# Performance work log

Measured on AMD Instinct MI355X. Metric: run time of the kernel, lower is better.

## Reference

```python
import jax, jax.numpy as jnp
import numpy as np
from jax import lax

EPS = 1e-7  # keras K.epsilon()
DN = ('NHWC', 'HWIO', 'NHWC')


def _box_avg(z, k):
    """Depthwise k x k box filter with SAME padding, scaled by 1/(k*k*C).
    Matches tf.nn.depthwise_conv2d with a ones/(k*k*C) kernel, implemented
    separably (two 1D convs) for efficiency."""
    C = z.shape[-1]
    scale = 1.0 / (k * k * C)  # note: keras code divides by full kernel size incl. C
    kh = jnp.ones((k, 1, 1, C), z.dtype)
    kw = jnp.ones((1, k, 1, C), z.dtype)
    z = lax.conv_general_dilated(z, kh, (1, 1), 'SAME',
                                 dimension_numbers=DN, feature_group_count=C)
    z = lax.conv_general_dilated(z, kw, (1, 1), 'SAME',
                                 dimension_numbers=DN, feature_group_count=C)
    return z * scale


def setup_inputs() -> dict:
    key = jax.random.key(0)
    x = jax.random.normal(key, (8, 1024, 1024, 2), dtype=jnp.float32)
    return {"x": x, "filter_size": 61}


def reference(x, filter_size):
    k = int(filter_size)
    # norm_method == 'std':
    out = x - _box_avg(x, k)                       # local mean-subtract
    c1 = _box_avg(out, k)
    c2 = _box_avg(out * out, k)
    std = jnp.sqrt(c2 - c1 * c1) + EPS             # local window std
    return out / std
```

## Files before the change

### kernel.cpp

```cpp
#include <hip/hip_runtime.h>
#include <math.h>

#define NB 8
#define HH 1024
#define WW 1024
#define CC 2
#define RAD 30
#define KS 61
#define ROWSZ (WW * CC)
#define IMGSZ (HH * ROWSZ)
#define STR (ROWSZ / 2)
#define NCOL2 (NB * STR)
#define VSEGH 64
#define VNSEG (HH / VSEGH)
#define EPSV 1e-7f
#define SCALEV (1.0f / (float)(KS * KS * CC))

__global__ __launch_bounds__(256) void vbox_kernel(const float* __restrict__ in,
                                                   float* __restrict__ out) {
    int tid = blockIdx.x * 256 + threadIdx.x;
    int col = tid & (NCOL2 - 1);
    int seg = tid >> 13;
    int n = col / STR;
    int wc = col & (STR - 1);
    const float2* ip = (const float2*)(in + (size_t)n * IMGSZ) + wc;
    float2* op = (float2*)(out + (size_t)n * IMGSZ) + wc;
    int h0 = seg * VSEGH;
    float Sx = 0.f, Sy = 0.f;
    int lo = h0 - RAD; if (lo < 0) lo = 0;
    int hiex = h0 + RAD;
    int h = lo;
    for (; h + 4 <= hiex; h += 4) {
        float2 v0 = ip[(h + 0) * STR];
        float2 v1 = ip[(h + 1) * STR];
        float2 v2 = ip[(h + 2) * STR];
        float2 v3 = ip[(h + 3) * STR];
        Sx += v0.x + v1.x + v2.x + v3.x;
        Sy += v0.y + v1.y + v2.y + v3.y;
    }
    for (; h < hiex; ++h) { float2 v = ip[h * STR]; Sx += v.x; Sy += v.y; }
    for (int ho = h0; ho < h0 + VSEGH; ho += 4) {
        float2 a[4], b[4];
        #pragma unroll
        for (int i = 0; i < 4; ++i) {
            int ha = ho + i + RAD;
            a[i] = (ha < HH) ? ip[ha * STR] : make_float2(0.f, 0.f);
        }
        #pragma unroll
        for (int i = 0; i < 4; ++i) {
            int hb = ho + i - RAD;
            b[i] = (hb >= 0) ? ip[hb * STR] : make_float2(0.f, 0.f);
        }
        #pragma unroll
        for (int i = 0; i < 4; ++i) {
            Sx += a[i].x; Sy += a[i].y;
            op[(ho + i) * STR] = make_float2(Sx, Sy);
            Sx -= b[i].x; Sy -= b[i].y;
        }
    }
}

__global__ __launch_bounds__(256) void vbox2_kernel(const float* __restrict__ in,
                                                    float* __restrict__ o1,
                                                    float* __restrict__ o2) {
    int tid = blockIdx.x * 256 + threadIdx.x;
    int col = tid & (NCOL2 - 1);
    int seg = tid >> 13;
    int n = col / STR;
    int wc = col & (STR - 1);
    const float2* ip = (const float2*)(in + (size_t)n * IMGSZ) + wc;
    float2* p1 = (float2*)(o1 + (size_t)n * IMGSZ) + wc;
    float2* p2 = (float2*)(o2 + (size_t)n * IMGSZ) + wc;
    int h0 = seg * VSEGH;
    float Sx = 0.f, Sy = 0.f, Qx = 0.f, Qy = 0.f;
    int lo = h0 - RAD; if (lo < 0) lo = 0;
    int hiex = h0 + RAD;
    int h = lo;
    for (; h + 4 <= hiex; h += 4) {
        float2 v0 = ip[(h + 0) * STR];
        float2 v1 = ip[(h + 1) * STR];
        float2 v2 = ip[(h + 2) * STR];
        float2 v3 = ip[(h + 3) * STR];
        Sx += v0.x + v1.x + v2.x + v3.x;
        Sy += v0.y + v1.y + v2.y + v3.y;
        Qx += v0.x * v0.x + v1.x * v1.x + v2.x * v2.x + v3.x * v3.x;
        Qy += v0.y * v0.y + v1.y * v1.y + v2.y * v2.y + v3.y * v3.y;
    }
    for (; h < hiex; ++h) {
        float2 v = ip[h * STR];
        Sx += v.x; Sy += v.y; Qx += v.x * v.x; Qy += v.y * v.y;
    }
    for (int ho = h0; ho < h0 + VSEGH; ho += 4) {
        float2 a[4], b[4];
        #pragma unroll
        for (int i = 0; i < 4; ++i) {
            int ha = ho + i + RAD;
            a[i] = (ha < HH) ? ip[ha * STR] : make_float2(0.f, 0.f);
        }
        #pragma unroll
        for (int i = 0; i < 4; ++i) {
            int hb = ho + i - RAD;
            b[i] = (hb >= 0) ? ip[hb * STR] : make_float2(0.f, 0.f);
        }
        #pragma unroll
        for (int i = 0; i < 4; ++i) {
            Sx += a[i].x; Sy += a[i].y;
            Qx += a[i].x * a[i].x; Qy += a[i].y * a[i].y;
            p1[(ho + i) * STR] = make_float2(Sx, Sy);
            p2[(ho + i) * STR] = make_float2(Qx, Qy);
            Sx -= b[i].x; Sy -= b[i].y;
            Qx -= b[i].x * b[i].x; Qy -= b[i].y * b[i].y;
        }
    }
}

__device__ inline float wave_incl_scan(float v) {
    int lane = threadIdx.x & 63;
    #pragma unroll
    for (int d = 1; d < 64; d <<= 1) {
        float o = __shfl_up(v, d, 64);
        if (lane >= d) v += o;
    }
    return v;
}

__global__ __launch_bounds__(256) void hbox_sub_kernel(const float* __restrict__ vsum,
                                                       const float* __restrict__ x,
                                                       float* __restrict__ out) {
    __shared__ float ch[2][WW];
    __shared__ float wtot[4];
    int t = threadIdx.x;
    size_t g = (size_t)blockIdx.x * ROWSZ;
    const float2* vrow = (const float2*)(vsum + g);
    #pragma unroll
    for (int i = 0; i < 4; ++i) {
        int w = t + 256 * i;
        float2 v = vrow[w];
        ch[0][w] = v.x; ch[1][w] = v.y;
    }
    __syncthreads();
    int c = t >> 7, j = t & 127, base = j * 8;
    float v[8]; float run = 0.f;
    #pragma unroll
    for (int i = 0; i < 8; ++i) { run += ch[c][base + i]; v[i] = run; }
    float incl = wave_incl_scan(run);
    int wid = t >> 6;
    if ((t & 63) == 63) wtot[wid] = incl;
    __syncthreads();
    float off = incl - run;
    if (wid & 1) off += wtot[wid - 1];
    #pragma unroll
    for (int i = 0; i < 8; ++i) ch[c][base + i] = off + v[i];
    __syncthreads();
    #pragma unroll
    for (int i = 0; i < 8; ++i) {
        int e = t + 256 * i;
        int w = e >> 1, cc2 = e & 1;
        int hi = w + RAD; if (hi > WW - 1) hi = WW - 1;
        float s = ch[cc2][hi];
        int lo2 = w - RAD - 1;
        if (lo2 >= 0) s -= ch[cc2][lo2];
        out[g + e] = x[g + e] - SCALEV * s;
    }
}

__global__ __launch_bounds__(256) void hbox_final_kernel(const float* __restrict__ s1v,
                                                         const float* __restrict__ s2v,
                                                         float* __restrict__ out) {
    __shared__ float ch[4][WW];
    int t = threadIdx.x;
    size_t g = (size_t)blockIdx.x * ROWSZ;
    const float2* arow = (const float2*)(s1v + g);
    const float2* brow = (const float2*)(s2v + g);
    #pragma unroll
    for (int i = 0; i < 4; ++i) {
        int w = t + 256 * i;
        float2 a = arow[w]; ch[0][w] = a.x; ch[1][w] = a.y;
        float2 b = brow[w]; ch[2][w] = b.x; ch[3][w] = b.y;
    }
    __syncthreads();
    int a = t >> 6, j = t & 63, base = j * 16;
    float v[16]; float run = 0.f;
    #pragma unroll
    for (int i = 0; i < 16; ++i) { run += ch[a][base + i]; v[i] = run; }
    float incl = wave_incl_scan(run);
    float off = incl - run;
    #pragma unroll
    for (int i = 0; i < 16; ++i) ch[a][base + i] = off + v[i];
    __syncthreads();
    #pragma unroll
    for (int i = 0; i < 8; ++i) {
        int e = t + 256 * i;
        int w = e >> 1, cc2 = e & 1;
        int hi = w + RAD; if (hi > WW - 1) hi = WW - 1;
        int lo2 = w - RAD - 1;
        float s1 = ch[cc2][hi];
        float s2 = ch[2 + cc2][hi];
        if (lo2 >= 0) { s1 -= ch[cc2][lo2]; s2 -= ch[2 + cc2][lo2]; }
        float c1 = SCALEV * s1;
        float c2 = SCALEV * s2;
        float var = c2 - c1 * c1;
        float stdv = sqrtf(fmaxf(var, 0.f)) + EPSV;
        out[g + e] = out[g + e] / stdv;
    }
}

extern "C" void kernel_launch(void* const* d_in, const int* in_sizes, int n_in,
                              void* d_out, int out_size, void* d_ws, size_t ws_size,
                              hipStream_t stream) {
    const float* x = (const float*)d_in[0];
    float* out = (float*)d_out;
    float* wsf = (float*)d_ws;
    float* V1 = wsf;
    float* V3 = wsf + (size_t)NB * IMGSZ;

    vbox_kernel<<<(NCOL2 * VNSEG) / 256, 256, 0, stream>>>(x, V1);
    hbox_sub_kernel<<<NB * HH, 256, 0, stream>>>(V1, x, out);
    vbox2_kernel<<<(NCOL2 * VNSEG) / 256, 256, 0, stream>>>(out, V1, V3);
    hbox_final_kernel<<<NB * HH, 256, 0, stream>>>(V1, V3, out);
}
```

Measured before the change: 239.9 us.

## Vectorize box-filter passes to float4 and pad shared memory to avoid conflicts

The vertical running-sum kernels now use float4 accesses, so each thread handles four floats. Segments are shortened to 32 rows, which keeps thread count similar and adds more warmup overhead per segment. Interior segments get a branch-free path with no boundary checks. The horizontal scan kernels load and store float4 and pad their shared-memory rows (one extra slot per 8) to reduce bank conflicts; this adds index arithmetic and replaces the interleaved access pattern.

```diff
diff --git a/kernel.cpp b/kernel.cpp
--- a/kernel.cpp
+++ b/kernel.cpp
@@ -9,53 +9,84 @@
 #define KS 61
 #define ROWSZ (WW * CC)
 #define IMGSZ (HH * ROWSZ)
-#define STR (ROWSZ / 2)
-#define NCOL2 (NB * STR)
-#define VSEGH 64
+#define STR4 (ROWSZ / 4)
+#define NCOL4 (NB * STR4)
+#define VSEGH 32
 #define VNSEG (HH / VSEGH)
 #define EPSV 1e-7f
 #define SCALEV (1.0f / (float)(KS * KS * CC))
+#define PDW (WW + WW / 8)
+#define PD(i) ((i) + ((i) >> 3))
+
+__device__ __forceinline__ float4 f4add(float4 a, float4 b) {
+    return make_float4(a.x + b.x, a.y + b.y, a.z + b.z, a.w + b.w);
+}
+__device__ __forceinline__ float4 f4sub(float4 a, float4 b) {
+    return make_float4(a.x - b.x, a.y - b.y, a.z - b.z, a.w - b.w);
+}
+__device__ __forceinline__ float4 f4fma(float4 a, float4 b, float4 c) {
+    return make_float4(fmaf(a.x, b.x, c.x), fmaf(a.y, b.y, c.y),
+                       fmaf(a.z, b.z, c.z), fmaf(a.w, b.w, c.w));
+}
 
 __global__ __launch_bounds__(256) void vbox_kernel(const float* __restrict__ in,
                                                    float* __restrict__ out) {
     int tid = blockIdx.x * 256 + threadIdx.x;
-    int col = tid & (NCOL2 - 1);
-    int seg = tid >> 13;
-    int n = col / STR;
-    int wc = col & (STR - 1);
-    const float2* ip = (const float2*)(in + (size_t)n * IMGSZ) + wc;
-    float2* op = (float2*)(out + (size_t)n * IMGSZ) + wc;
+    int col = tid & (NCOL4 - 1);
+    int seg = tid >> 12;
+    int n = col >> 9;
+    int w4 = col & (STR4 - 1);
+    const float4* ip = (const float4*)(in + (size_t)n * IMGSZ) + w4;
+    float4* op = (float4*)(out + (size_t)n * IMGSZ) + w4;
     int h0 = seg * VSEGH;
-    float Sx = 0.f, Sy = 0.f;
+    float4 S = make_float4(0.f, 0.f, 0.f, 0.f);
     int lo = h0 - RAD; if (lo < 0) lo = 0;
     int hiex = h0 + RAD;
     int h = lo;
     for (; h + 4 <= hiex; h += 4) {
-        float2 v0 = ip[(h + 0) * STR];
-        float2 v1 = ip[(h + 1) * STR];
-        float2 v2 = ip[(h + 2) * STR];
-        float2 v3 = ip[(h + 3) * STR];
-        Sx += v0.x + v1.x + v2.x + v3.x;
-        Sy += v0.y + v1.y + v2.y + v3.y;
-    }
-    for (; h < hiex; ++h) { float2 v = ip[h * STR]; Sx += v.x; Sy += v.y; }
-    for (int ho = h0; ho < h0 + VSEGH; ho += 4) {
-        float2 a[4], b[4];
-        #pragma unroll
-        for (int i = 0; i < 4; ++i) {
-            int ha = ho + i + RAD;
-            a[i] = (ha < HH) ? ip[ha * STR] : make_float2(0.f, 0.f);
-        }
-        #pragma unroll
-        for (int i = 0; i < 4; ++i) {
-            int hb = ho + i - RAD;
-            b[i] = (hb >= 0) ? ip[hb * STR] : make_float2(0.f, 0.f);
-        }
-        #pragma unroll
-        for (int i = 0; i < 4; ++i) {
-            Sx += a[i].x; Sy += a[i].y;
-            op[(ho + i) * STR] = make_float2(Sx, Sy);
-            Sx -= b[i].x; Sy -= b[i].y;
+        float4 v0 = ip[(h + 0) * STR4];
+        float4 v1 = ip[(h + 1) * STR4];
+        float4 v2 = ip[(h + 2) * STR4];
+        float4 v3 = ip[(h + 3) * STR4];
+        S = f4add(S, f4add(f4add(v0, v1), f4add(v2, v3)));
+    }
+    for (; h < hiex; ++h) S = f4add(S, ip[h * STR4]);
+
+    if (seg != 0 && seg != VNSEG - 1) {
+        for (int ho = h0; ho < h0 + VSEGH; ho += 4) {
+            float4 a0 = ip[(ho + 0 + RAD) * STR4];
+            float4 a1 = ip[(ho + 1 + RAD) * STR4];
+            float4 a2 = ip[(ho + 2 + RAD) * STR4];
+            float4 a3 = ip[(ho + 3 + RAD) * STR4];
+            float4 b0 = ip[(ho + 0 - RAD) * STR4];
+            float4 b1 = ip[(ho + 1 - RAD) * STR4];
+            float4 b2 = ip[(ho + 2 - RAD) * STR4];
+            float4 b3 = ip[(ho + 3 - RAD) * STR4];
+            S = f4add(S, a0); op[(ho + 0) * STR4] = S; S = f4sub(S, b0);
+            S = f4add(S, a1); op[(ho + 1) * STR4] = S; S = f4sub(S, b1);
+            S = f4add(S, a2); op[(ho + 2) * STR4] = S; S = f4sub(S, b2);
+            S = f4add(S, a3); op[(ho + 3) * STR4] = S; S = f4sub(S, b3);
+        }
+    } else {
+        const float4 Z = make_float4(0.f, 0.f, 0.f, 0.f);
+        for (int ho = h0; ho < h0 + VSEGH; ho += 4) {
+            float4 a[4], b[4];
+            #pragma unroll
+            for (int i = 0; i < 4; ++i) {
+                int ha = ho + i + RAD;
+                a[i] = (ha < HH) ? ip[ha * STR4] : Z;
+            }
+            #pragma unroll
+            for (int i = 0; i < 4; ++i) {
+                int hb = ho + i - RAD;
+                b[i] = (hb >= 0) ? ip[hb * STR4] : Z;
+            }
+            #pragma unroll
+            for (int i = 0; i < 4; ++i) {
+                S = f4add(S, a[i]);
+                op[(ho + i) * STR4] = S;
+                S = f4sub(S, b[i]);
+            }
         }
     }
 }
@@ -64,52 +95,78 @@
                                                     float* __restrict__ o1,
                                                     float* __restrict__ o2) {
     int tid = blockIdx.x * 256 + threadIdx.x;
-    int col = tid & (NCOL2 - 1);
-    int seg = tid >> 13;
-    int n = col / STR;
-    int wc = col & (STR - 1);
-    const float2* ip = (const float2*)(in + (size_t)n * IMGSZ) + wc;
-    float2* p1 = (float2*)(o1 + (size_t)n * IMGSZ) + wc;
-    float2* p2 = (float2*)(o2 + (size_t)n * IMGSZ) + wc;
+    int col = tid & (NCOL4 - 1);
+    int seg = tid >> 12;
+    int n = col >> 9;
+    int w4 = col & (STR4 - 1);
+    const float4* ip = (const float4*)(in + (size_t)n * IMGSZ) + w4;
+    float4* p1 = (float4*)(o1 + (size_t)n * IMGSZ) + w4;
+    float4* p2 = (float4*)(o2 + (size_t)n * IMGSZ) + w4;
     int h0 = seg * VSEGH;
-    float Sx = 0.f, Sy = 0.f, Qx = 0.f, Qy = 0.f;
+    float4 S = make_float4(0.f, 0.f, 0.f, 0.f);
+    float4 Q = make_float4(0.f, 0.f, 0.f, 0.f);
     int lo = h0 - RAD; if (lo < 0) lo = 0;
     int hiex = h0 + RAD;
     int h = lo;
     for (; h + 4 <= hiex; h += 4) {
-        float2 v0 = ip[(h + 0) * STR];
-        float2 v1 = ip[(h + 1) * STR];
-        float2 v2 = ip[(h + 2) * STR];
-        float2 v3 = ip[(h + 3) * STR];
-        Sx += v0.x + v1.x + v2.x + v3.x;
-        Sy += v0.y + v1.y + v2.y + v3.y;
-        Qx += v0.x * v0.x + v1.x * v1.x + v2.x * v2.x + v3.x * v3.x;
-        Qy += v0.y * v0.y + v1.y * v1.y + v2.y * v2.y + v3.y * v3.y;
+        float4 v0 = ip[(h + 0) * STR4];
+        float4 v1 = ip[(h + 1) * STR4];
+        float4 v2 = ip[(h + 2) * STR4];
+        float4 v3 = ip[(h + 3) * STR4];
+        S = f4add(S, f4add(f4add(v0, v1), f4add(v2, v3)));
+        Q = f4fma(v0, v0, Q); Q = f4fma(v1, v1, Q);
+        Q = f4fma(v2, v2, Q); Q = f4fma(v3, v3, Q);
     }
     for (; h < hiex; ++h) {
-        float2 v = ip[h * STR];
-        Sx += v.x; Sy += v.y; Qx += v.x * v.x; Qy += v.y * v.y;
-    }
-    for (int ho = h0; ho < h0 + VSEGH; ho += 4) {
-        float2 a[4], b[4];
-        #pragma unroll
-        for (int i = 0; i < 4; ++i) {
-            int ha = ho + i + RAD;
-            a[i] = (ha < HH) ? ip[ha * STR] : make_float2(0.f, 0.f);
-        }
-        #pragma unroll
-        for (int i = 0; i < 4; ++i) {
-            int hb = ho + i - RAD;
-            b[i] = (hb >= 0) ? ip[hb * STR] : make_float2(0.f, 0.f);
-        }
-        #pragma unroll
-        for (int i = 0; i < 4; ++i) {
-            Sx += a[i].x; Sy += a[i].y;
-            Qx += a[i].x * a[i].x; Qy += a[i].y * a[i].y;
-            p1[(ho + i) * STR] = make_float2(Sx, Sy);
-            p2[(ho + i) * STR] = make_float2(Qx, Qy);
-            Sx -= b[i].x; Sy -= b[i].y;
-            Qx -= b[i].x * b[i].x; Qy -= b[i].y * b[i].y;
+        float4 v = ip[h * STR4];
+        S = f4add(S, v); Q = f4fma(v, v, Q);
+    }
+
+    if (seg != 0 && seg != VNSEG - 1) {
+        for (int ho = h0; ho < h0 + VSEGH; ho += 4) {
+            float4 a0 = ip[(ho + 0 + RAD) * STR4];
+            float4 a1 = ip[(ho + 1 + RAD) * STR4];
+            float4 a2 = ip[(ho + 2 + RAD) * STR4];
+            float4 a3 = ip[(ho + 3 + RAD) * STR4];
+            float4 b0 = ip[(ho + 0 - RAD) * STR4];
+            float4 b1 = ip[(ho + 1 - RAD) * STR4];
+            float4 b2 = ip[(ho + 2 - RAD) * STR4];
+            float4 b3 = ip[(ho + 3 - RAD) * STR4];
+            S = f4add(S, a0); Q = f4fma(a0, a0, Q);
+            p1[(ho + 0) * STR4] = S; p2[(ho + 0) * STR4] = Q;
+            S = f4sub(S, b0); Q = make_float4(fmaf(-b0.x, b0.x, Q.x), fmaf(-b0.y, b0.y, Q.y), fmaf(-b0.z, b0.z, Q.z), fmaf(-b0.w, b0.w, Q.w));
+            S = f4add(S, a1); Q = f4fma(a1, a1, Q);
+            p1[(ho + 1) * STR4] = S; p2[(ho + 1) * STR4] = Q;
+            S = f4sub(S, b1); Q = make_float4(fmaf(-b1.x, b1.x, Q.x), fmaf(-b1.y, b1.y, Q.y), fmaf(-b1.z, b1.z, Q.z), fmaf(-b1.w, b1.w, Q.w));
+            S = f4add(S, a2); Q = f4fma(a2, a2, Q);
+            p1[(ho + 2) * STR4] = S; p2[(ho + 2) * STR4] = Q;
+            S = f4sub(S, b2); Q = make_float4(fmaf(-b2.x, b2.x, Q.x), fmaf(-b2.y, b2.y, Q.y), fmaf(-b2.z, b2.z, Q.z), fmaf(-b2.w, b2.w, Q.w));
+            S = f4add(S, a3); Q = f4fma(a3, a3, Q);
+            p1[(ho + 3) * STR4] = S; p2[(ho + 3) * STR4] = Q;
+            S = f4sub(S, b3); Q = make_float4(fmaf(-b3.x, b3.x, Q.x), fmaf(-b3.y, b3.y, Q.y), fmaf(-b3.z, b3.z, Q.z), fmaf(-b3.w, b3.w, Q.w));
+        }
+    } else {
+        const float4 Z = make_float4(0.f, 0.f, 0.f, 0.f);
+        for (int ho = h0; ho < h0 + VSEGH; ho += 4) {
+            float4 a[4], b[4];
+            #pragma unroll
+            for (int i = 0; i < 4; ++i) {
+                int ha = ho + i + RAD;
+                a[i] = (ha < HH) ? ip[ha * STR4] : Z;
+            }
+            #pragma unroll
+            for (int i = 0; i < 4; ++i) {
+                int hb = ho + i - RAD;
+                b[i] = (hb >= 0) ? ip[hb * STR4] : Z;
+            }
+            #pragma unroll
+            for (int i = 0; i < 4; ++i) {
+                S = f4add(S, a[i]); Q = f4fma(a[i], a[i], Q);
+                p1[(ho + i) * STR4] = S; p2[(ho + i) * STR4] = Q;
+                S = f4sub(S, b[i]);
+                Q = make_float4(fmaf(-b[i].x, b[i].x, Q.x), fmaf(-b[i].y, b[i].y, Q.y),
+                                fmaf(-b[i].z, b[i].z, Q.z), fmaf(-b[i].w, b[i].w, Q.w));
+            }
         }
     }
 }
@@ -127,22 +184,23 @@
 __global__ __launch_bounds__(256) void hbox_sub_kernel(const float* __restrict__ vsum,
                                                        const float* __restrict__ x,
                                                        float* __restrict__ out) {
-    __shared__ float ch[2][WW];
+    __shared__ float ch[2][PDW];
     __shared__ float wtot[4];
     int t = threadIdx.x;
     size_t g = (size_t)blockIdx.x * ROWSZ;
-    const float2* vrow = (const float2*)(vsum + g);
-    #pragma unroll
-    for (int i = 0; i < 4; ++i) {
-        int w = t + 256 * i;
-        float2 v = vrow[w];
-        ch[0][w] = v.x; ch[1][w] = v.y;
+    const float4* vrow = (const float4*)(vsum + g);
+    #pragma unroll
+    for (int i = 0; i < 2; ++i) {
+        int j = t + 256 * i;
+        float4 v = vrow[j];
+        ch[0][PD(2 * j)] = v.x;     ch[1][PD(2 * j)] = v.y;
+        ch[0][PD(2 * j + 1)] = v.z; ch[1][PD(2 * j + 1)] = v.w;
     }
     __syncthreads();
     int c = t >> 7, j = t & 127, base = j * 8;
     float v[8]; float run = 0.f;
     #pragma unroll
-    for (int i = 0; i < 8; ++i) { run += ch[c][base + i]; v[i] = run; }
+    for (int i = 0; i < 8; ++i) { run += ch[c][PD(base + i)]; v[i] = run; }
     float incl = wave_incl_scan(run);
     int wid = t >> 6;
     if ((t & 63) == 63) wtot[wid] = incl;
@@ -150,58 +208,89 @@
     float off = incl - run;
     if (wid & 1) off += wtot[wid - 1];
     #pragma unroll
-    for (int i = 0; i < 8; ++i) ch[c][base + i] = off + v[i];
-    __syncthreads();
-    #pragma unroll
-    for (int i = 0; i < 8; ++i) {
-        int e = t + 256 * i;
-        int w = e >> 1, cc2 = e & 1;
-        int hi = w + RAD; if (hi > WW - 1) hi = WW - 1;
-        float s = ch[cc2][hi];
-        int lo2 = w - RAD - 1;
-        if (lo2 >= 0) s -= ch[cc2][lo2];
-        out[g + e] = x[g + e] - SCALEV * s;
+    for (int i = 0; i < 8; ++i) ch[c][PD(base + i)] = off + v[i];
+    __syncthreads();
+    const float4* xrow = (const float4*)(x + g);
+    float4* orow = (float4*)(out + g);
+    #pragma unroll
+    for (int i = 0; i < 2; ++i) {
+        int jj = t + 256 * i;
+        int w0 = 2 * jj, w1 = 2 * jj + 1;
+        int hi0 = w0 + RAD; if (hi0 > WW - 1) hi0 = WW - 1;
+        int hi1 = w1 + RAD; if (hi1 > WW - 1) hi1 = WW - 1;
+        int lo0 = w0 - RAD - 1, lo1 = w1 - RAD - 1;
+        float s00 = ch[0][PD(hi0)], s10 = ch[1][PD(hi0)];
+        if (lo0 >= 0) { s00 -= ch[0][PD(lo0)]; s10 -= ch[1][PD(lo0)]; }
+        float s01 = ch[0][PD(hi1)], s11 = ch[1][PD(hi1)];
+        if (lo1 >= 0) { s01 -= ch[0][PD(lo1)]; s11 -= ch[1][PD(lo1)]; }
+        float4 xv = xrow[jj];
+        float4 o;
+        o.x = xv.x - SCALEV * s00; o.y = xv.y - SCALEV * s10;
+        o.z = xv.z - SCALEV * s01; o.w = xv.w - SCALEV * s11;
+        orow[jj] = o;
     }
 }
 
 __global__ __launch_bounds__(256) void hbox_final_kernel(const float* __restrict__ s1v,
                                                          const float* __restrict__ s2v,
                                                          float* __restrict__ out) {
-    __shared__ float ch[4][WW];
+    __shared__ float ch[4][PDW];
     int t = threadIdx.x;
     size_t g = (size_t)blockIdx.x * ROWSZ;
-    const float2* arow = (const float2*)(s1v + g);
-    const float2* brow = (const float2*)(s2v + g);
-    #pragma unroll
-    for (int i = 0; i < 4; ++i) {
-        int w = t + 256 * i;
-        float2 a = arow[w]; ch[0][w] = a.x; ch[1][w] = a.y;
-        float2 b = brow[w]; ch[2][w] = b.x; ch[3][w] = b.y;
+    const float4* arow = (const float4*)(s1v + g);
+    const float4* brow = (const float4*)(s2v + g);
+    #pragma unroll
+    for (int i = 0; i < 2; ++i) {
+        int j = t + 256 * i;
+        float4 a = arow[j];
+        ch[0][PD(2 * j)] = a.x;     ch[1][PD(2 * j)] = a.y;
+        ch[0][PD(2 * j + 1)] = a.z; ch[1][PD(2 * j + 1)] = a.w;
+        float4 b = brow[j];
+        ch[2][PD(2 * j)] = b.x;     ch[3][PD(2 * j)] = b.y;
+        ch[2][PD(2 * j + 1)] = b.z; ch[3][PD(2 * j + 1)] = b.w;
     }
     __syncthreads();
     int a = t >> 6, j = t & 63, base = j * 16;
     float v[16]; float run = 0.f;
     #pragma unroll
-    for (int i = 0; i < 16; ++i) { run += ch[a][base + i]; v[i] = run; }
+    for (int i = 0; i < 16; ++i) { run += ch[a][PD(base + i)]; v[i] = run; }
     float incl = wave_incl_scan(run);
     float off = incl - run;
     #pragma unroll
-    for (int i = 0; i < 16; ++i) ch[a][base + i] = off + v[i];
-    __syncthreads();
-    #pragma unroll
-    for (int i = 0; i < 8; ++i) {
-        int e = t + 256 * i;
-        int w = e >> 1, cc2 = e & 1;
-        int hi = w + RAD; if (hi > WW - 1) hi = WW - 1;
-        int lo2 = w - RAD - 1;
-        float s1 = ch[cc2][hi];
-        float s2 = ch[2 + cc2][hi];
-        if (lo2 >= 0) { s1 -= ch[cc2][lo2]; s2 -= ch[2 + cc2][lo2]; }
-        float c1 = SCALEV * s1;
-        float c2 = SCALEV * s2;
-        float var = c2 - c1 * c1;
-        float stdv = sqrtf(fmaxf(var, 0.f)) + EPSV;
-        out[g + e] = out[g + e] / stdv;
+    for (int i = 0; i < 16; ++i) ch[a][PD(base + i)] = off + v[i];
+    __syncthreads();
+    float4* orow = (float4*)(out + g);
+    #pragma unroll
+    for (int i = 0; i < 2; ++i) {
+        int jj = t + 256 * i;
+        int w0 = 2 * jj, w1 = 2 * jj + 1;
+        int hi0 = w0 + RAD; if (hi0 > WW - 1) hi0 = WW - 1;
+        int hi1 = w1 + RAD; if (hi1 > WW - 1) hi1 = WW - 1;
+        int lo0 = w0 - RAD - 1, lo1 = w1 - RAD - 1;
+        float s1a = ch[0][PD(hi0)], s1b = ch[1][PD(hi0)];
+        float s2a = ch[2][PD(hi0)], s2b = ch[3][PD(hi0)];
+        if (lo0 >= 0) {
+            s1a -= ch[0][PD(lo0)]; s1b -= ch[1][PD(lo0)];
+            s2a -= ch[2][PD(lo0)]; s2b -= ch[3][PD(lo0)];
+        }
+        float s1c = ch[0][PD(hi1)], s1d = ch[1][PD(hi1)];
+        float s2c = ch[2][PD(hi1)], s2d = ch[3][PD(hi1)];
+        if (lo1 >= 0) {
+            s1c -= ch[0][PD(lo1)]; s1d -= ch[1][PD(lo1)];
+            s2c -= ch[2][PD(lo1)]; s2d -= ch[3][PD(lo1)];
+        }
+        float4 ov = orow[jj];
+        float c1, c2, var;
+        float4 r;
+        c1 = SCALEV * s1a; c2 = SCALEV * s2a; var = c2 - c1 * c1;
+        r.x = ov.x / (sqrtf(fmaxf(var, 0.f)) + EPSV);
+        c1 = SCALEV * s1b; c2 = SCALEV * s2b; var = c2 - c1 * c1;
+        r.y = ov.y / (sqrtf(fmaxf(var, 0.f)) + EPSV);
+        c1 = SCALEV * s1c; c2 = SCALEV * s2c; var = c2 - c1 * c1;
+        r.z = ov.z / (sqrtf(fmaxf(var, 0.f)) + EPSV);
+        c1 = SCALEV * s1d; c2 = SCALEV * s2d; var = c2 - c1 * c1;
+        r.w = ov.w / (sqrtf(fmaxf(var, 0.f)) + EPSV);
+        orow[jj] = r;
     }
 }
 
@@ -214,8 +303,8 @@
     float* V1 = wsf;
     float* V3 = wsf + (size_t)NB * IMGSZ;
 
-    vbox_kernel<<<(NCOL2 * VNSEG) / 256, 256, 0, stream>>>(x, V1);
+    vbox_kernel<<<(NCOL4 * VNSEG) / 256, 256, 0, stream>>>(x, V1);
     hbox_sub_kernel<<<NB * HH, 256, 0, stream>>>(V1, x, out);
-    vbox2_kernel<<<(NCOL2 * VNSEG) / 256, 256, 0, stream>>>(out, V1, V3);
+    vbox2_kernel<<<(NCOL4 * VNSEG) / 256, 256, 0, stream>>>(out, V1, V3);
     hbox_final_kernel<<<NB * HH, 256, 0, stream>>>(V1, V3, out);
 }
```

Result: slower. 251.7 us (+4.9%).
